# Performance work log

Hardware: AMD Instinct MI355X
Metric: run time of the kernel (lower is better)

## Reference

```python
import jax, jax.numpy as jnp
import numpy as np

N_NODES = 50000
N_EDGES = 800000
D_IN = 128
D_HID = 128
D_OUT = 1


def gcn_layer(x, W, b, src, dst, n_nodes):
    """PyG GCNConv: h = XW; out = D^{-1/2}(A+I)D^{-1/2} h + b.

    deg[i] = in_degree(i) + 1 (self loop). Self-loop contribution is added
    directly as h * deg^{-1} instead of materializing extra edges.
    """
    h = x @ W  # [N, d_out]
    deg = jnp.zeros((n_nodes,), dtype=x.dtype).at[dst].add(1.0) + 1.0
    dinv = jax.lax.rsqrt(deg)  # deg^{-1/2}
    norm = (dinv[src] * dinv[dst])[:, None]  # [E, 1]
    agg = jnp.zeros_like(h).at[dst].add(h[src] * norm)  # scatter-add messages
    agg = agg + h * (dinv * dinv)[:, None]  # self loops: deg^{-1} * h
    return agg + b


def setup_inputs() -> dict:
    key = jax.random.key(0)
    ks = jax.random.split(key, 8)
    x = jax.random.normal(ks[0], (N_NODES, D_IN), dtype=jnp.float32)
    edge_index = jax.random.randint(ks[1], (2, N_EDGES), 0, N_NODES, dtype=jnp.int64 if jax.config.jax_enable_x64 else jnp.int32)
    s1 = 1.0 / np.sqrt(D_IN)
    s2 = 1.0 / np.sqrt(D_HID)
    W1 = jax.random.uniform(ks[2], (D_IN, D_HID), jnp.float32, -s1, s1)
    b1 = jnp.zeros((D_HID,), jnp.float32)
    W2 = jax.random.uniform(ks[3], (D_HID, D_HID), jnp.float32, -s2, s2)
    b2 = jnp.zeros((D_HID,), jnp.float32)
    Wr = jax.random.uniform(ks[4], (D_HID, D_OUT), jnp.float32, -s2, s2)
    br = jax.random.uniform(ks[5], (D_OUT,), jnp.float32, -s2, s2)
    return {"x": x, "edge_index": edge_index, "W1": W1, "b1": b1,
            "W2": W2, "b2": b2, "Wr": Wr, "br": br}


def reference(x, edge_index, W1, b1, W2, b2, Wr, br):
    src, dst = edge_index[0], edge_index[1]
    n = x.shape[0]
    h = jax.nn.relu(gcn_layer(x, W1, b1, src, dst, n))
    h = jax.nn.relu(gcn_layer(h, W2, b2, src, dst, n))
    return h @ Wr + br  # [N, output_dim]
```

## Files before the change

### kernel.cpp

```cpp
#include <hip/hip_runtime.h>
#include <hip/hip_fp16.h>
#include <cstdint>
#include <cstddef>


constexpr int DIM = 128;
#define BSH 6
#define BIN_EPT 13
#define FT 8
#define FSH 13
#define STAGE 2048

typedef __attribute__((ext_vector_type(8))) short bf16x8;
typedef __attribute__((ext_vector_type(4))) float f32x4;

__device__ __forceinline__ short bf16h(float x) {
    unsigned u = __float_as_uint(x);
    return (short)((u + 0x7FFFu + ((u >> 16) & 1u)) >> 16);
}
__device__ __forceinline__ float bf16f(short h) {
    return __uint_as_float(((unsigned)(unsigned short)h) << 16);
}

__global__ __launch_bounds__(256) void k_hist(const int* __restrict__ dst,
                                              int* __restrict__ bcount, int E, int nb) {
    __shared__ int h[1024];
    for (int i = threadIdx.x; i < nb; i += 256) h[i] = 0;
    __syncthreads();
    int stride = gridDim.x * 256;
    for (int e = blockIdx.x * 256 + threadIdx.x; e < E; e += stride)
        atomicAdd(&h[dst[e] >> BSH], 1);
    __syncthreads();
    for (int i = threadIdx.x; i < nb; i += 256) {
        int c = h[i];
        if (c) atomicAdd(&bcount[i], c);
    }
}

__global__ __launch_bounds__(1024) void k_bscan(const int* __restrict__ bcount,
                                                int* __restrict__ bptr,
                                                int* __restrict__ bcur, int nb, int E) {
    __shared__ int s[1024];
    int t = threadIdx.x;
    int v = (t < nb) ? bcount[t] : 0;
    s[t] = v;
    __syncthreads();
    for (int off = 1; off < 1024; off <<= 1) {
        int u = (t >= off) ? s[t - off] : 0;
        __syncthreads();
        s[t] += u;
        __syncthreads();
    }
    if (t < nb) { int ex = s[t] - v; bptr[t] = ex; bcur[t] = ex; }
    if (t == 0) bptr[nb] = E;
}

__global__ __launch_bounds__(256) void k_bin(const int* __restrict__ src,
                                             const int* __restrict__ dst,
                                             int* __restrict__ bcur,
                                             unsigned* __restrict__ pairs,
                                             int E, int nb) {
    __shared__ int h[1024];
    __shared__ int base[1024];
    for (int i = threadIdx.x; i < nb; i += 256) h[i] = 0;
    __syncthreads();

    int e0 = blockIdx.x * 256 * BIN_EPT;
    unsigned u[BIN_EPT];
    int cnt = 0;
#pragma unroll
    for (int j = 0; j < BIN_EPT; j++) {
        int e = e0 + j * 256 + threadIdx.x;
        if (e < E) {
            int d = dst[e];
            u[j] = ((unsigned)d << 16) | (unsigned)src[e];
            atomicAdd(&h[d >> BSH], 1);
            cnt = j + 1;
        }
    }
    __syncthreads();
    for (int i = threadIdx.x; i < nb; i += 256) {
        int c = h[i];
        base[i] = c ? atomicAdd(&bcur[i], c) : 0;
    }
    __syncthreads();
#pragma unroll
    for (int j = 0; j < BIN_EPT; j++) {
        if (j < cnt) {
            int pos = atomicAdd(&base[u[j] >> 22], 1);
            pairs[pos] = u[j];
        }
    }
}

__global__ __launch_bounds__(256) void k_fill2(const unsigned* __restrict__ pairs,
                                               const int* __restrict__ bptr,
                                               int* __restrict__ row_ptr,
                                               float* __restrict__ dinv,
                                               int* __restrict__ col,
                                               int N, int nb, int E) {
    __shared__ unsigned sp[STAGE];
    __shared__ int lcnt[64 * FT];
    int b = blockIdx.x;
    int node0 = b << BSH;
    int beg = bptr[b], end = bptr[b + 1];
    int cnt = end - beg;
    bool useStage = (cnt <= STAGE);

    for (int i = threadIdx.x; i < 64 * FT; i += 256) lcnt[i] = 0;
    __syncthreads();

    for (int i = threadIdx.x; i < cnt; i += 256) {
        unsigned u = pairs[beg + i];
        if (useStage) sp[i] = u;
        atomicAdd(&lcnt[((u >> 16) & 63) * FT + ((u & 0xffffu) >> FSH)], 1);
    }
    __syncthreads();

    if (threadIdx.x < 64) {
        int t = threadIdx.x;
        int c[FT]; int sum = 0;
#pragma unroll
        for (int f = 0; f < FT; f++) { c[f] = lcnt[t * FT + f]; sum += c[f]; }
        int x = sum;
#pragma unroll
        for (int off = 1; off < 64; off <<= 1) {
            int y = __shfl_up(x, off, 64);
            if (t >= off) x += y;
        }
        int nodebase = beg + x - sum;
        int node = node0 + t;
        if (node < N) {
            row_ptr[node] = nodebase;
            dinv[node] = rsqrtf((float)sum + 1.0f);
        }
        int run = nodebase;
#pragma unroll
        for (int f = 0; f < FT; f++) { lcnt[t * FT + f] = run; run += c[f]; }
        if (b == nb - 1 && t == 0) row_ptr[N] = E;
    }
    __syncthreads();

    for (int i = threadIdx.x; i < cnt; i += 256) {
        unsigned u = useStage ? sp[i] : pairs[beg + i];
        unsigned s = u & 0xffffu;
        int pos = atomicAdd(&lcnt[((u >> 16) & 63) * FT + (s >> FSH)], 1);
        col[pos] = (int)s;
    }
}

__global__ __launch_bounds__(256) void k_wfrag2(const float* __restrict__ W1,
                                                const float* __restrict__ W2,
                                                short* __restrict__ Bh1,
                                                short* __restrict__ Bl1,
                                                short* __restrict__ Bh2,
                                                short* __restrict__ Bl2,
                                                int* __restrict__ bcount, int nb) {
    int idx = blockIdx.x * 256 + threadIdx.x;
    if (idx < nb) bcount[idx] = 0;
    const float* W = (idx < 16384) ? W1 : W2;
    short* Bh = (idx < 16384) ? Bh1 : Bh2;
    short* Bl = (idx < 16384) ? Bl1 : Bl2;
    int id = idx & 16383;
    int j  = id & 7;
    int l  = (id >> 3) & 63;
    int ks = (id >> 9) & 3;
    int nt = id >> 11;
    int k   = ks * 32 + ((l >> 4) * 8) + j;
    int c   = nt * 16 + (l & 15);
    float w = W[k * 128 + c];
    short h = bf16h(w);
    Bh[id] = h;
    Bl[id] = bf16h(w - bf16f(h));
}

__device__ __forceinline__ void load8(const float* p, float* v) {
    float4 a = *(const float4*)p;
    float4 b = *(const float4*)(p + 4);
    v[0] = a.x; v[1] = a.y; v[2] = a.z; v[3] = a.w;
    v[4] = b.x; v[5] = b.y; v[6] = b.z; v[7] = b.w;
}
__device__ __forceinline__ void load8(const __half* p, float* v) {
    float4 a = *(const float4*)p;
    const __half2* h = (const __half2*)&a;
#pragma unroll
    for (int i = 0; i < 4; i++) {
        float2 f = __half22float2(h[i]);
        v[2 * i] = f.x; v[2 * i + 1] = f.y;
    }
}

template <typename T>
__global__ __launch_bounds__(256) void k_mm(const T* __restrict__ X,
                                            const short* __restrict__ Bhp,
                                            const short* __restrict__ Blp,
                                            const float* __restrict__ dinv,
                                            __half* __restrict__ Hh, int N) {
    int gw   = (blockIdx.x * 256 + threadIdx.x) >> 6;
    int lane = threadIdx.x & 63;
    int row0 = gw * 16;
    if (row0 >= N) return;

    int arow = row0 + (lane & 15);
    if (arow >= N) arow = N - 1;
    const T* Xp = X + (size_t)arow * DIM + ((lane >> 4) * 8);

    bf16x8 Ah[4], Al[4];
#pragma unroll
    for (int ks = 0; ks < 4; ks++) {
        float v[8];
        load8(Xp + ks * 32, v);
        bf16x8 h, lo;
#pragma unroll
        for (int j = 0; j < 8; j++) {
            short hh = bf16h(v[j]);
            h[j] = hh;
            lo[j] = bf16h(v[j] - bf16f(hh));
        }
        Ah[ks] = h;
        Al[ks] = lo;
    }

    const bf16x8* BH = (const bf16x8*)Bhp;
    const bf16x8* BL = (const bf16x8*)Blp;

    f32x4 acc[8];
#pragma unroll
    for (int nt = 0; nt < 8; nt++) {
        f32x4 c = {0.f, 0.f, 0.f, 0.f};
#pragma unroll
        for (int ks = 0; ks < 4; ks++) {
            bf16x8 bh = BH[(nt * 4 + ks) * 64 + lane];
            bf16x8 bl = BL[(nt * 4 + ks) * 64 + lane];
            c = __builtin_amdgcn_mfma_f32_16x16x32_bf16(Ah[ks], bh, c, 0, 0, 0);
            c = __builtin_amdgcn_mfma_f32_16x16x32_bf16(Al[ks], bh, c, 0, 0, 0);
            c = __builtin_amdgcn_mfma_f32_16x16x32_bf16(Ah[ks], bl, c, 0, 0, 0);
        }
        acc[nt] = c;
    }

    int rb = row0 + ((lane >> 4) * 4);
    int cb = lane & 15;
#pragma unroll
    for (int r = 0; r < 4; r++) {
        if (rb + r < N) {
            float dv = dinv[rb + r];
            __half* out = Hh + (size_t)(rb + r) * DIM + cb;
#pragma unroll
            for (int nt = 0; nt < 8; nt++)
                out[nt * 16] = __float2half(acc[nt][r] * dv);
        }
    }
}

__device__ __forceinline__ float2 agg_row(const __half2* __restrict__ Hh,
                                          const int* __restrict__ row_ptr,
                                          const int* __restrict__ col,
                                          const float* __restrict__ dinv,
                                          const float* __restrict__ B,
                                          int wid, int lane) {
    int beg = __builtin_amdgcn_readfirstlane(row_ptr[wid]);
    int end = __builtin_amdgcn_readfirstlane(row_ptr[wid + 1]);
    const __half2* Hl = Hh + lane;
    float2 s0f = __half22float2(Hl[(size_t)wid * 64]);
    float ax = s0f.x, ay = s0f.y;
    float bx = 0.f, by = 0.f, cx = 0.f, cy = 0.f, dx = 0.f, dy = 0.f;

    int e = beg;
    for (; e + 16 <= end; e += 16) {
        __half2 g[16];
#pragma unroll
        for (int j = 0; j < 16; j++) g[j] = Hl[(size_t)col[e + j] * 64];
#pragma unroll
        for (int j = 0; j < 16; j += 4) {
            float2 f0 = __half22float2(g[j + 0]);
            float2 f1 = __half22float2(g[j + 1]);
            float2 f2 = __half22float2(g[j + 2]);
            float2 f3 = __half22float2(g[j + 3]);
            ax += f0.x; ay += f0.y;  bx += f1.x; by += f1.y;
            cx += f2.x; cy += f2.y;  dx += f3.x; dy += f3.y;
        }
    }
    for (; e + 8 <= end; e += 8) {
        __half2 g[8];
#pragma unroll
        for (int j = 0; j < 8; j++) g[j] = Hl[(size_t)col[e + j] * 64];
#pragma unroll
        for (int j = 0; j < 8; j += 4) {
            float2 f0 = __half22float2(g[j + 0]);
            float2 f1 = __half22float2(g[j + 1]);
            float2 f2 = __half22float2(g[j + 2]);
            float2 f3 = __half22float2(g[j + 3]);
            ax += f0.x; ay += f0.y;  bx += f1.x; by += f1.y;
            cx += f2.x; cy += f2.y;  dx += f3.x; dy += f3.y;
        }
    }
    for (; e + 4 <= end; e += 4) {
        __half2 g0 = Hl[(size_t)col[e + 0] * 64];
        __half2 g1 = Hl[(size_t)col[e + 1] * 64];
        __half2 g2 = Hl[(size_t)col[e + 2] * 64];
        __half2 g3 = Hl[(size_t)col[e + 3] * 64];
        float2 f0 = __half22float2(g0), f1 = __half22float2(g1);
        float2 f2 = __half22float2(g2), f3 = __half22float2(g3);
        ax += f0.x; ay += f0.y;  bx += f1.x; by += f1.y;
        cx += f2.x; cy += f2.y;  dx += f3.x; dy += f3.y;
    }
    for (; e < end; e++) {
        float2 f = __half22float2(Hl[(size_t)col[e] * 64]);
        ax += f.x; ay += f.y;
    }
    ax += bx + cx + dx;
    ay += by + cy + dy;

    float di = dinv[wid];
    float2 b = *(const float2*)(B + lane * 2);
    return make_float2(fmaf(di, ax, b.x), fmaf(di, ay, b.y));
}

__global__ __launch_bounds__(256) void k_agg(const __half2* __restrict__ Hh,
                                             const int* __restrict__ row_ptr,
                                             const int* __restrict__ col,
                                             const float* __restrict__ dinv,
                                             const float* __restrict__ B,
                                             __half2* __restrict__ O, int N) {
    int wid = (blockIdx.x * 256 + threadIdx.x) >> 6;
    int lane = threadIdx.x & 63;
    if (wid >= N) return;
    float2 r = agg_row(Hh, row_ptr, col, dinv, B, wid, lane);
    O[(size_t)wid * 64 + lane] = __floats2half2_rn(fmaxf(r.x, 0.f), fmaxf(r.y, 0.f));
}

__global__ __launch_bounds__(256) void k_agg_out(const __half2* __restrict__ Hh,
                                                 const int* __restrict__ row_ptr,
                                                 const int* __restrict__ col,
                                                 const float* __restrict__ dinv,
                                                 const float* __restrict__ B,
                                                 const float* __restrict__ Wr,
                                                 const float* __restrict__ br,
                                                 float* __restrict__ out, int N) {
    int wid = (blockIdx.x * 256 + threadIdx.x) >> 6;
    int lane = threadIdx.x & 63;
    if (wid >= N) return;
    float2 r = agg_row(Hh, row_ptr, col, dinv, B, wid, lane);
    float2 w = *(const float2*)(Wr + lane * 2);
    float v = fmaxf(r.x, 0.f) * w.x + fmaxf(r.y, 0.f) * w.y;
#pragma unroll
    for (int off = 32; off > 0; off >>= 1) v += __shfl_down(v, off, 64);
    if (lane == 0) out[wid] = v + br[0];
}

extern "C" void kernel_launch(void* const* d_in, const int* in_sizes, int n_in,
                              void* d_out, int out_size, void* d_ws, size_t ws_size,
                              hipStream_t stream) {
    const float* x  = (const float*)d_in[0];
    const int*   ei = (const int*)d_in[1];
    const float* W1 = (const float*)d_in[2];
    const float* b1 = (const float*)d_in[3];
    const float* W2 = (const float*)d_in[4];
    const float* b2 = (const float*)d_in[5];
    const float* Wr = (const float*)d_in[6];
    const float* br = (const float*)d_in[7];

    const int N = in_sizes[0] / DIM;
    const int E = in_sizes[1] / 2;
    const int* src = ei;
    const int* dst = ei + E;
    const int NB = (N + 63) >> BSH;

    char* p = (char*)d_ws;
    auto alloc = [&](size_t bytes) -> void* {
        void* r = (void*)p;
        p += (bytes + 255) & ~(size_t)255;
        return r;
    };
    __half*   Hh      = (__half*)alloc((size_t)N * DIM * 2);
    __half*   A1      = (__half*)alloc((size_t)N * DIM * 2);
    float*    dinv    = (float*)alloc((size_t)N * 4);
    int*      row_ptr = (int*)alloc((size_t)(N + 1) * 4);
    int*      bcount  = (int*)alloc((size_t)NB * 4);
    int*      bptr    = (int*)alloc((size_t)(NB + 1) * 4);
    int*      bcur    = (int*)alloc((size_t)NB * 4);
    unsigned* pairs   = (unsigned*)alloc((size_t)E * 4);
    int*      col     = (int*)alloc((size_t)E * 4);
    short*    Bh1     = (short*)alloc(16384 * 2);
    short*    Bl1     = (short*)alloc(16384 * 2);
    short*    Bh2     = (short*)alloc(16384 * 2);
    short*    Bl2     = (short*)alloc(16384 * 2);
    (void)ws_size; (void)n_in;

    k_wfrag2<<<128, 256, 0, stream>>>(W1, W2, Bh1, Bl1, Bh2, Bl2, bcount, NB);

    k_hist<<<256, 256, 0, stream>>>(dst, bcount, E, NB);
    k_bscan<<<1, 1024, 0, stream>>>(bcount, bptr, bcur, NB, E);
    const int binb = (E + 256 * BIN_EPT - 1) / (256 * BIN_EPT);
    k_bin<<<binb, 256, 0, stream>>>(src, dst, bcur, pairs, E, NB);
    k_fill2<<<NB, 256, 0, stream>>>(pairs, bptr, row_ptr, dinv, col, N, NB, E);

    const int mmb = ((N + 15) / 16 + 3) / 4;
    const int ab  = (N * 64 + 255) / 256;

    k_mm<float><<<mmb, 256, 0, stream>>>(x, Bh1, Bl1, dinv, Hh, N);
    k_agg<<<ab, 256, 0, stream>>>((const __half2*)Hh, row_ptr, col, dinv, b1,
                                  (__half2*)A1, N);
    k_mm<__half><<<mmb, 256, 0, stream>>>(A1, Bh2, Bl2, dinv, Hh, N);
    k_agg_out<<<ab, 256, 0, stream>>>((const __half2*)Hh, row_ptr, col, dinv, b2,
                                      Wr, br, (float*)d_out, N);
}
```

Before: 137.6 us.

## Fuse weight prep with histogram, use per-block partials, vectorize edge loads

Merges the weight-fragment conversion and the destination histogram into one kernel, which removes a launch. Each block now writes its own partial histogram, so the zero-init and global atomics go away, and the scan kernel sums 128 partials per bucket. The histogram and binning kernels read src/dst as int4, and the binning items-per-thread drops from 13 to 12 so the count divides by four. The costs are a serial 128-iteration reduction inside the single-block scan, and int4 loads of src/dst that assume 16-byte alignment.

```diff
diff --git a/kernel.cpp b/kernel.cpp
--- a/kernel.cpp
+++ b/kernel.cpp
@@ -6,7 +6,8 @@
 
 constexpr int DIM = 128;
 #define BSH 6
-#define BIN_EPT 13
+#define HB 128
+#define BIN_EPT 12
 #define FT 8
 #define FSH 13
 #define STAGE 2048
@@ -22,27 +23,58 @@
     return __uint_as_float(((unsigned)(unsigned short)h) << 16);
 }
 
-__global__ __launch_bounds__(256) void k_hist(const int* __restrict__ dst,
-                                              int* __restrict__ bcount, int E, int nb) {
+__global__ __launch_bounds__(256) void k_prep(const float* __restrict__ W1,
+                                              const float* __restrict__ W2,
+                                              short* __restrict__ Bh1,
+                                              short* __restrict__ Bl1,
+                                              short* __restrict__ Bh2,
+                                              short* __restrict__ Bl2,
+                                              const int* __restrict__ dst,
+                                              int* __restrict__ h_part,
+                                              int E, int nb) {
+    {
+        int idx = blockIdx.x * 256 + threadIdx.x;
+        const float* W = (idx < 16384) ? W1 : W2;
+        short* Bh = (idx < 16384) ? Bh1 : Bh2;
+        short* Bl = (idx < 16384) ? Bl1 : Bl2;
+        int id = idx & 16383;
+        int j  = id & 7;
+        int l  = (id >> 3) & 63;
+        int ks = (id >> 9) & 3;
+        int nt = id >> 11;
+        int k  = ks * 32 + ((l >> 4) * 8) + j;
+        int c  = nt * 16 + (l & 15);
+        float w = W[k * 128 + c];
+        short h = bf16h(w);
+        Bh[id] = h;
+        Bl[id] = bf16h(w - bf16f(h));
+    }
     __shared__ int h[1024];
-    for (int i = threadIdx.x; i < nb; i += 256) h[i] = 0;
-    __syncthreads();
-    int stride = gridDim.x * 256;
-    for (int e = blockIdx.x * 256 + threadIdx.x; e < E; e += stride)
-        atomicAdd(&h[dst[e] >> BSH], 1);
-    __syncthreads();
-    for (int i = threadIdx.x; i < nb; i += 256) {
-        int c = h[i];
-        if (c) atomicAdd(&bcount[i], c);
-    }
-}
-
-__global__ __launch_bounds__(1024) void k_bscan(const int* __restrict__ bcount,
+    for (int i = threadIdx.x; i < 1024; i += 256) h[i] = 0;
+    __syncthreads();
+    int E4 = E >> 2;
+    for (int v = blockIdx.x * 256 + threadIdx.x; v < E4; v += HB * 256) {
+        int4 d4 = *(const int4*)(dst + v * 4);
+        atomicAdd(&h[d4.x >> BSH], 1);
+        atomicAdd(&h[d4.y >> BSH], 1);
+        atomicAdd(&h[d4.z >> BSH], 1);
+        atomicAdd(&h[d4.w >> BSH], 1);
+    }
+    if (blockIdx.x == 0 && threadIdx.x < (E & 3))
+        atomicAdd(&h[dst[E4 * 4 + threadIdx.x] >> BSH], 1);
+    __syncthreads();
+    for (int i = threadIdx.x; i < nb; i += 256)
+        h_part[blockIdx.x * 1024 + i] = h[i];
+}
+
+__global__ __launch_bounds__(1024) void k_bscan(const int* __restrict__ h_part,
                                                 int* __restrict__ bptr,
                                                 int* __restrict__ bcur, int nb, int E) {
     __shared__ int s[1024];
     int t = threadIdx.x;
-    int v = (t < nb) ? bcount[t] : 0;
+    int v = 0;
+    if (t < nb)
+        for (int b = 0; b < HB; b++) v += h_part[b * 1024 + t];
     s[t] = v;
     __syncthreads();
     for (int off = 1; off < 1024; off <<= 1) {
@@ -69,13 +101,31 @@
     unsigned u[BIN_EPT];
     int cnt = 0;
 #pragma unroll
-    for (int j = 0; j < BIN_EPT; j++) {
-        int e = e0 + j * 256 + threadIdx.x;
-        if (e < E) {
-            int d = dst[e];
-            u[j] = ((unsigned)d << 16) | (unsigned)src[e];
-            atomicAdd(&h[d >> BSH], 1);
-            cnt = j + 1;
+    for (int j = 0; j < BIN_EPT / 4; j++) {
+        int b4 = e0 + j * 1024 + threadIdx.x * 4;
+        if (b4 + 4 <= E) {
+            int4 s4 = *(const int4*)(src + b4);
+            int4 d4 = *(const int4*)(dst + b4);
+            u[4 * j + 0] = ((unsigned)d4.x << 16) | (unsigned)s4.x;
+            u[4 * j + 1] = ((unsigned)d4.y << 16) | (unsigned)s4.y;
+            u[4 * j + 2] = ((unsigned)d4.z << 16) | (unsigned)s4.z;
+            u[4 * j + 3] = ((unsigned)d4.w << 16) | (unsigned)s4.w;
+            atomicAdd(&h[d4.x >> BSH], 1);
+            atomicAdd(&h[d4.y >> BSH], 1);
+            atomicAdd(&h[d4.z >> BSH], 1);
+            atomicAdd(&h[d4.w >> BSH], 1);
+            cnt = 4 * j + 4;
+        } else {
+#pragma unroll
+            for (int k = 0; k < 4; k++) {
+                int e = b4 + k;
+                if (e < E) {
+                    int d = dst[e];
+                    u[4 * j + k] = ((unsigned)d << 16) | (unsigned)src[e];
+                    atomicAdd(&h[d >> BSH], 1);
+                    cnt = 4 * j + k + 1;
+                }
+            }
         }
     }
     __syncthreads();
@@ -147,31 +197,6 @@
         int pos = atomicAdd(&lcnt[((u >> 16) & 63) * FT + (s >> FSH)], 1);
         col[pos] = (int)s;
     }
-}
-
-__global__ __launch_bounds__(256) void k_wfrag2(const float* __restrict__ W1,
-                                                const float* __restrict__ W2,
-                                                short* __restrict__ Bh1,
-                                                short* __restrict__ Bl1,
-                                                short* __restrict__ Bh2,
-                                                short* __restrict__ Bl2,
-                                                int* __restrict__ bcount, int nb) {
-    int idx = blockIdx.x * 256 + threadIdx.x;
-    if (idx < nb) bcount[idx] = 0;
-    const float* W = (idx < 16384) ? W1 : W2;
-    short* Bh = (idx < 16384) ? Bh1 : Bh2;
-    short* Bl = (idx < 16384) ? Bl1 : Bl2;
-    int id = idx & 16383;
-    int j  = id & 7;
-    int l  = (id >> 3) & 63;
-    int ks = (id >> 9) & 3;
-    int nt = id >> 11;
-    int k   = ks * 32 + ((l >> 4) * 8) + j;
-    int c   = nt * 16 + (l & 15);
-    float w = W[k * 128 + c];
-    short h = bf16h(w);
-    Bh[id] = h;
-    Bl[id] = bf16h(w - bf16f(h));
 }
 
 __device__ __forceinline__ void load8(const float* p, float* v) {
@@ -377,7 +402,7 @@
     __half*   A1      = (__half*)alloc((size_t)N * DIM * 2);
     float*    dinv    = (float*)alloc((size_t)N * 4);
     int*      row_ptr = (int*)alloc((size_t)(N + 1) * 4);
-    int*      bcount  = (int*)alloc((size_t)NB * 4);
+    int*      h_part  = (int*)alloc((size_t)HB * 1024 * 4);
     int*      bptr    = (int*)alloc((size_t)(NB + 1) * 4);
     int*      bcur    = (int*)alloc((size_t)NB * 4);
     unsigned* pairs   = (unsigned*)alloc((size_t)E * 4);
@@ -388,10 +413,8 @@
     short*    Bl2     = (short*)alloc(16384 * 2);
     (void)ws_size; (void)n_in;
 
-    k_wfrag2<<<128, 256, 0, stream>>>(W1, W2, Bh1, Bl1, Bh2, Bl2, bcount, NB);
-
-    k_hist<<<256, 256, 0, stream>>>(dst, bcount, E, NB);
-    k_bscan<<<1, 1024, 0, stream>>>(bcount, bptr, bcur, NB, E);
+    k_prep<<<HB, 256, 0, stream>>>(W1, W2, Bh1, Bl1, Bh2, Bl2, dst, h_part, E, NB);
+    k_bscan<<<1, 1024, 0, stream>>>(h_part, bptr, bcur, NB, E);
     const int binb = (E + 256 * BIN_EPT - 1) / (256 * BIN_EPT);
     k_bin<<<binb, 256, 0, stream>>>(src, dst, bcur, pairs, E, NB);
     k_fill2<<<NB, 256, 0, stream>>>(pairs, bptr, row_ptr, dinv, col, N, NB, E);
```

After: 131.4 us, median of 2. -4.5%, faster.
